# Optimization experiments

Measured on AMD Instinct MI355X. Metric: run time of the kernel, lower is better.

## Reference

```python
import jax, jax.numpy as jnp
import numpy as np

N_NODES = 20000   # num_of_nodes + 1 (incl. prediction node)
FEAT = 256        # in_features == hidden_features == out_features
N_LAYERS = 2
ALPHA = 0.2       # LeakyReLU negative slope
V_OBS = 512       # observed codes per patient
D_H = np.sqrt(FEAT * 1.0)  # sqrt(hidden_features * num_of_heads), n_heads=1
EPS = 1e-6


def _fc_edges(nodes):
    # torch: source = nodes.repeat(1, n); dest = each node repeated n times
    n = len(nodes)
    return np.stack([np.tile(nodes, n), np.repeat(nodes, n)]).astype(np.int64)


def setup_inputs() -> dict:
    key = jax.random.key(0)
    ks = jax.random.split(key, 16)
    rng = np.random.default_rng(0)
    obs = np.sort(rng.choice(np.arange(1, N_NODES - 1), size=V_OBS, replace=False))
    input_edges = jnp.asarray(_fc_edges(obs))
    obs_out = np.concatenate([obs, [N_NODES - 1]])  # add prediction node
    output_edges = jnp.asarray(_fc_edges(obs_out))

    s = 0.02
    embed = s * jax.random.normal(ks[0], (N_NODES, FEAT), jnp.float32)
    embed = embed.at[0].set(0.0)  # padding_idx=0
    return {
        "embed": embed,
        "W_w": s * jax.random.normal(ks[1], (N_LAYERS, FEAT, FEAT), jnp.float32),
        "W_b": s * jax.random.normal(ks[2], (N_LAYERS, FEAT), jnp.float32),
        "a": s * jax.random.normal(ks[3], (N_LAYERS, 2 * FEAT), jnp.float32),
        "ln_a": jnp.ones((N_LAYERS, FEAT), jnp.float32),
        "ln_b": jnp.zeros((N_LAYERS, FEAT), jnp.float32),
        "Wo_w": s * jax.random.normal(ks[4], (FEAT, FEAT), jnp.float32),
        "Wo_b": s * jax.random.normal(ks[5], (FEAT,), jnp.float32),
        "ao": s * jax.random.normal(ks[6], (2 * FEAT,), jnp.float32),
        "lno_a": jnp.ones((FEAT,), jnp.float32),
        "lno_b": jnp.zeros((FEAT,), jnp.float32),
        "lin_w": s * jax.random.normal(ks[7], (FEAT, FEAT), jnp.float32),
        "lin_b": s * jax.random.normal(ks[8], (FEAT,), jnp.float32),
        "param_w": s * jax.random.normal(ks[9], (2 * FEAT, FEAT), jnp.float32),
        "param_b": s * jax.random.normal(ks[10], (2 * FEAT,), jnp.float32),
        "out1_w": s * jax.random.normal(ks[11], (FEAT, FEAT), jnp.float32),
        "out1_b": s * jax.random.normal(ks[12], (FEAT,), jnp.float32),
        "out2_w": s * jax.random.normal(ks[13], (1, FEAT), jnp.float32),
        "out2_b": s * jax.random.normal(ks[14], (1,), jnp.float32),
        "input_edges": input_edges,
        "output_edges": output_edges,
    }


def _attention(x, edges, Ww, Wb, avec):
    # d = Linear(x): (N, H)
    d = x @ Ww.T + Wb
    H = d.shape[1]
    # a . [d_src ; d_dst] == (d @ a_left)[src] + (d @ a_right)[dst]  (cheaper, same math)
    s_node = d @ avec[:H]
    t_node = d @ avec[H:]
    score = s_node[edges[0]] + t_node[edges[1]]                  # (E,)
    e = jnp.exp(jax.nn.leaky_relu(score, ALPHA) / D_H)           # unnormalized attn
    n = x.shape[0]
    rowsum = jax.ops.segment_sum(e, edges[0], num_segments=n)   # (N,)
    agg = jax.ops.segment_sum(e[:, None] * d[edges[1]], edges[0], num_segments=n)
    zero = rowsum == 0
    # rows with no in-edges get an identity self-edge of weight 1 and rowsum 1
    agg = agg + jnp.where(zero[:, None], d, 0.0)
    return agg / jnp.where(zero, 1.0, rowsum)[:, None]


def _layernorm(x, g, b):
    m = x.mean(-1, keepdims=True)
    s = jnp.std(x, axis=-1, ddof=1, keepdims=True)  # torch std: unbiased
    return g * (x - m) / (s + EPS) + b


def reference(embed, W_w, W_b, a, ln_a, ln_b, Wo_w, Wo_b, ao, lno_a, lno_b,
              lin_w, lin_b, param_w, param_b, out1_w, out1_b, out2_w, out2_b,
              input_edges, output_edges):
    h = embed  # embedding lookup of arange(N) == the full table
    for l in range(N_LAYERS):  # in_att stack, concat=True, n_heads=1: ffn = LN -> ELU
        h = jax.nn.elu(_layernorm(_attention(h, input_edges, W_w[l], W_b[l], a[l]),
                                  ln_a[l], ln_b[l]))
    # variational layer (eval mode: reparameterize returns mu)
    hp = (h @ param_w.T + param_b).reshape(-1, 2, FEAT)
    h = hp[:, 0, :]  # mu
    # out_att: concat=False, mean over 1 head; ffn = LN -> ReLU -> Linear
    g = _attention(h, output_edges, Wo_w, Wo_b, ao)
    g = jax.nn.relu(_layernorm(g, lno_a, lno_b)) @ lin_w.T + lin_b
    # out_layer on prediction node: ReLU -> Linear -> ReLU -> Linear(->1)
    z = jax.nn.relu(g[-1])
    z = jax.nn.relu(z @ out1_w.T + out1_b)
    logit = z @ out2_w.T + out2_b  # (1,)
    return logit
```

## Files before the change

### kernel.cpp

```cpp
#include <hip/hip_runtime.h>
#include <hip/hip_bf16.h>

#define FEAT 256
#define NOBS 512
#define NOUT 513
#define GAT_ALPHA 0.2f
#define INV_DH (1.0f / 16.0f)
#define LN_EPS 1e-6f


__device__ __forceinline__ float b2f(unsigned short u) {
    union { float f; unsigned v; } x;
    x.v = ((unsigned)u) << 16;
    return x.f;
}

__device__ __forceinline__ float loadv(const void* p, long idx, int isbf) {
    if (isbf) return b2f(((const unsigned short*)p)[idx]);
    return ((const float*)p)[idx];
}

__device__ __forceinline__ float4 load4(const void* p, long idx, int isbf) {
    if (isbf) {
        ushort4 u = *(const ushort4*)((const unsigned short*)p + idx);
        return make_float4(b2f(u.x), b2f(u.y), b2f(u.z), b2f(u.w));
    }
    return *(const float4*)((const float*)p + idx);
}

__device__ __forceinline__ void detect(const void* w, const void* edges, int& isbf, int& estep) {
    const unsigned short* hb = (const unsigned short*)w;
    int sane = 0;
#pragma unroll
    for (int i = 0; i < 32; i += 2) {
        float a = fabsf(b2f(hb[i]));
        sane += (a > 1e-4f && a < 0.3f) ? 1 : 0;
    }
    isbf = (sane >= 8) ? 1 : 0;
    const int* ei = (const int*)edges;
    estep = (ei[1] == 0 && ei[3] == 0 && ei[5] == 0 && ei[7] == 0) ? 2 : 1;
}

__device__ __forceinline__ float wave_allreduce(float v) {
#pragma unroll
    for (int o = 1; o < 64; o <<= 1) v += __shfl_xor(v, o);
    return v;
}

__device__ __forceinline__ float block_sum256(float v, float* red) {
    __syncthreads();
    float s = v;
#pragma unroll
    for (int o = 32; o > 0; o >>= 1) s += __shfl_down(s, o);
    int lane = threadIdx.x & 63, wid = threadIdx.x >> 6;
    if (lane == 0) red[wid] = s;
    __syncthreads();
    return red[0] + red[1] + red[2] + red[3];
}

#define FV_AS0 0
#define FV_AS1 256
#define FV_AT0 512
#define FV_AT1 768
#define FV_WB0 1024
#define FV_WB1 1280
#define FV_LNA0 1536
#define FV_LNA1 1792
#define FV_LNB0 2048
#define FV_LNB1 2304
#define FV_WOB 2560
#define FV_AOS 2816
#define FV_AOT 3072
#define FV_LNOA 3328
#define FV_LNOB 3584
#define FV_LINB 3840
#define FV_PARB 4096
#define FV_O1B 4352
#define FV_O2W 4608
#define FV_O2B 4864

__global__ void k_prep(const void* embed, const void* W_w, const void* W_b, const void* a,
                       const void* ln_a, const void* ln_b, const void* Wo_w, const void* Wo_b,
                       const void* ao, const void* lno_a, const void* lno_b, const void* lin_w,
                       const void* lin_b, const void* param_w, const void* param_b,
                       const void* out1_w, const void* out1_b, const void* out2_w,
                       const void* out2_b, const void* oedges,
                       float* fv, float* packs, float* X, int* flags) {
    int isbf, estep;
    detect(W_w, oedges, isbf, estep);
    int b = blockIdx.x, tid = threadIdx.x;
    if (b < 96) {
        __shared__ float tile[64][65];
        int m = b >> 4, t = b & 15;
        int f0 = (t >> 2) << 6, k0 = (t & 3) << 6;
        const void* base;
        long eoff = 0;
        switch (m) {
            case 0: base = W_w; break;
            case 1: base = W_w; eoff = 65536; break;
            case 2: base = param_w; break;
            case 3: base = Wo_w; break;
            case 4: base = lin_w; break;
            default: base = out1_w; break;
        }
        int r = tid >> 2, cq = (tid & 3) << 4;
#pragma unroll
        for (int jj = 0; jj < 4; jj++) {
            float4 v = load4(base, eoff + (long)(f0 + r) * FEAT + k0 + cq + (jj << 2), isbf);
            tile[r][cq + (jj << 2) + 0] = v.x;
            tile[r][cq + (jj << 2) + 1] = v.y;
            tile[r][cq + (jj << 2) + 2] = v.z;
            tile[r][cq + (jj << 2) + 3] = v.w;
        }
        __syncthreads();
        int w = tid >> 6, lane = tid & 63;
        float4* pack = (float4*)(packs + (long)m * 65536);
#pragma unroll
        for (int it = 0; it < 4; it++) {
            int kk = ((w << 2) + it) << 2;
            float4 v = make_float4(tile[lane][kk], tile[lane][kk + 1],
                                   tile[lane][kk + 2], tile[lane][kk + 3]);
            int k4g = (k0 >> 2) + (w << 2) + it;
            pack[(k4g << 8) + f0 + lane] = v;
        }
    } else if (b < 96 + NOUT) {
        int i = b - 96;
        const int* oe = (const int*)oedges;
        long node = oe[(long)i * estep];
        X[(long)i * FEAT + tid] = loadv(embed, node * FEAT + tid, isbf);
    } else {
        int cid = b - 96 - NOUT;
        const void* s;
        long so = 0;
        float* d;
        int n = 256;
        switch (cid) {
            case 0:  s = a;       so = 0;   d = fv + FV_AS0;  break;
            case 1:  s = a;       so = 512; d = fv + FV_AS1;  break;
            case 2:  s = a;       so = 256; d = fv + FV_AT0;  break;
            case 3:  s = a;       so = 768; d = fv + FV_AT1;  break;
            case 4:  s = W_b;     so = 0;   d = fv + FV_WB0;  break;
            case 5:  s = W_b;     so = 256; d = fv + FV_WB1;  break;
            case 6:  s = ln_a;    so = 0;   d = fv + FV_LNA0; break;
            case 7:  s = ln_a;    so = 256; d = fv + FV_LNA1; break;
            case 8:  s = ln_b;    so = 0;   d = fv + FV_LNB0; break;
            case 9:  s = ln_b;    so = 256; d = fv + FV_LNB1; break;
            case 10: s = Wo_b;    so = 0;   d = fv + FV_WOB;  break;
            case 11: s = ao;      so = 0;   d = fv + FV_AOS;  break;
            case 12: s = ao;      so = 256; d = fv + FV_AOT;  break;
            case 13: s = lno_a;   so = 0;   d = fv + FV_LNOA; break;
            case 14: s = lno_b;   so = 0;   d = fv + FV_LNOB; break;
            case 15: s = lin_b;   so = 0;   d = fv + FV_LINB; break;
            case 16: s = param_b; so = 0;   d = fv + FV_PARB; break;
            case 17: s = out1_b;  so = 0;   d = fv + FV_O1B;  break;
            case 18: s = out2_w;  so = 0;   d = fv + FV_O2W;  break;
            default: s = out2_b;  so = 0;   d = fv + FV_O2B;  n = 1; break;
        }
        for (int idx = tid; idx < n; idx += FEAT) d[idx] = loadv(s, so + idx, isbf);
        if (cid == 19 && tid == 0) { flags[0] = isbf; flags[1] = estep; }
    }
}

template <bool WITH_ST, bool PWO>
__global__ void k_dense(const float* __restrict__ X, const float4* __restrict__ W1,
                        const float* __restrict__ b1, const float4* __restrict__ W2,
                        const float* __restrict__ b2v, const float* __restrict__ as_,
                        const float* __restrict__ at_, float* __restrict__ D,
                        float* S, float* T) {
    __shared__ __align__(16) float4 xs4[4][64];
    __shared__ __align__(16) float dsh[4][FEAT];
    int tid = threadIdx.x, lane = tid & 63, w = tid >> 6;
    int i0 = blockIdx.x << 2;
    int nr = NOUT - i0;
    if (nr > 4) nr = 4;
    if (w < nr) xs4[w][lane] = ((const float4*)(X + (long)(i0 + w) * FEAT))[lane];
    __syncthreads();
    float acc[4] = {0.f, 0.f, 0.f, 0.f};
#pragma unroll 4
    for (int k4 = 0; k4 < 64; k4++) {
        float4 wv = W1[(k4 << 8) + tid];
#pragma unroll
        for (int r = 0; r < 4; r++) {
            float4 xv = xs4[r][k4];
            acc[r] += xv.x * wv.x + xv.y * wv.y + xv.z * wv.z + xv.w * wv.w;
        }
    }
    float bb = b1[tid];
#pragma unroll
    for (int r = 0; r < 4; r++) acc[r] += bb;
    if (PWO) {
#pragma unroll
        for (int r = 0; r < 4; r++) dsh[r][tid] = acc[r];
        __syncthreads();
        float acc2[4] = {0.f, 0.f, 0.f, 0.f};
#pragma unroll 4
        for (int k4 = 0; k4 < 64; k4++) {
            float4 wv = W2[(k4 << 8) + tid];
#pragma unroll
            for (int r = 0; r < 4; r++) {
                float4 xv = ((const float4*)dsh[r])[k4];
                acc2[r] += xv.x * wv.x + xv.y * wv.y + xv.z * wv.z + xv.w * wv.w;
            }
        }
        float b2 = b2v[tid];
#pragma unroll
        for (int r = 0; r < 4; r++) acc[r] = acc2[r] + b2;
    }
#pragma unroll
    for (int r = 0; r < 4; r++)
        if (r < nr) D[(long)(i0 + r) * FEAT + tid] = acc[r];
    if (WITH_ST) {
        __syncthreads();
#pragma unroll
        for (int r = 0; r < 4; r++) dsh[r][tid] = acc[r];
        __syncthreads();
        if (w < nr) {
            float sv = 0.f, tv = 0.f;
#pragma unroll
            for (int q = 0; q < 4; q++) {
                float dv = dsh[w][lane + (q << 6)];
                sv += dv * as_[lane + (q << 6)];
                tv += dv * at_[lane + (q << 6)];
            }
            sv = wave_allreduce(sv);
            tv = wave_allreduce(tv);
            if (lane == 0) { S[i0 + w] = sv; T[i0 + w] = tv; }
        }
    }
}

__global__ void k_attn(const float* __restrict__ D, const float* __restrict__ S,
                       const float* __restrict__ T, const float* __restrict__ ga,
                       const float* __restrict__ gb, float* __restrict__ Xout) {
    __shared__ __align__(16) float e[4][NOBS];
    __shared__ __align__(16) float sacc[4][4][FEAT];
    __shared__ float rs[4];
    __shared__ float red[8];
    int tid = threadIdx.x, lane = tid & 63, w = tid >> 6;
    int bi = blockIdx.x;
    if (bi < 128) {
        int i0 = bi << 2;
#pragma unroll
        for (int r = 0; r < 4; r++) {
            float si = S[i0 + r];
#pragma unroll
            for (int h = 0; h < 2; h++) {
                int j = tid + (h << 8);
                float sc = si + T[j];
                sc = (sc > 0.f ? sc : GAT_ALPHA * sc) * INV_DH;
                e[r][j] = __expf(sc);
            }
        }
        __syncthreads();
        float p = 0.f;
#pragma unroll
        for (int q = 0; q < 8; q++) p += e[w][lane + (q << 6)];
        p = wave_allreduce(p);
        if (lane == 0) rs[w] = p;
        float4 a0 = make_float4(0.f, 0.f, 0.f, 0.f), a1 = a0, a2 = a0, a3 = a0;
#pragma unroll 4
        for (int jj = 0; jj < 128; jj++) {
            int j = (jj << 2) | w;
            float4 dv = *(const float4*)(D + (long)j * FEAT + (lane << 2));
            float e0 = e[0][j], e1 = e[1][j], e2 = e[2][j], e3 = e[3][j];
            a0.x += e0 * dv.x; a0.y += e0 * dv.y; a0.z += e0 * dv.z; a0.w += e0 * dv.w;
            a1.x += e1 * dv.x; a1.y += e1 * dv.y; a1.z += e1 * dv.z; a1.w += e1 * dv.w;
            a2.x += e2 * dv.x; a2.y += e2 * dv.y; a2.z += e2 * dv.z; a2.w += e2 * dv.w;
            a3.x += e3 * dv.x; a3.y += e3 * dv.y; a3.z += e3 * dv.z; a3.w += e3 * dv.w;
        }
        *(float4*)&sacc[w][0][lane << 2] = a0;
        *(float4*)&sacc[w][1][lane << 2] = a1;
        *(float4*)&sacc[w][2][lane << 2] = a2;
        *(float4*)&sacc[w][3][lane << 2] = a3;
        __syncthreads();
        float inv_rs = 1.f / rs[w];
        float v[4], m = 0.f;
#pragma unroll
        for (int q = 0; q < 4; q++) {
            int f = lane + (q << 6);
            v[q] = (sacc[0][w][f] + sacc[1][w][f] + sacc[2][w][f] + sacc[3][w][f]) * inv_rs;
            m += v[q];
        }
        m = wave_allreduce(m) * (1.f / FEAT);
        float var = 0.f;
#pragma unroll
        for (int q = 0; q < 4; q++) { v[q] -= m; var += v[q] * v[q]; }
        var = wave_allreduce(var) * (1.f / (FEAT - 1));
        float isd = 1.f / (sqrtf(var) + LN_EPS);
#pragma unroll
        for (int q = 0; q < 4; q++) {
            int f = lane + (q << 6);
            float y = ga[f] * v[q] * isd + gb[f];
            Xout[(long)(i0 + w) * FEAT + f] = (y > 0.f) ? y : (__expf(y) - 1.f);
        }
    } else {
        float val = D[(long)NOBS * FEAT + tid];
        float m = block_sum256(val, red) * (1.f / FEAT);
        float dv = val - m;
        float var = block_sum256(dv * dv, red) * (1.f / (FEAT - 1));
        float y = ga[tid] * dv / (sqrtf(var) + LN_EPS) + gb[tid];
        Xout[(long)NOBS * FEAT + tid] = (y > 0.f) ? y : (__expf(y) - 1.f);
    }
}

__global__ void k_aggout(const float* __restrict__ D, const float* __restrict__ S,
                         const float* __restrict__ T, float* partial, float* prsum) {
    __shared__ float es[16];
    __shared__ __align__(16) float wacc[4][FEAT];
    int tid = threadIdx.x, lane = tid & 63, w = tid >> 6;
    int b = blockIdx.x;
    float sN = S[NOUT - 1];
    if (b == 32) {
        float sc = sN + T[NOUT - 1];
        sc = (sc > 0.f ? sc : GAT_ALPHA * sc) * INV_DH;
        float ev = __expf(sc);
        partial[(long)b * FEAT + tid] = ev * D[(long)(NOUT - 1) * FEAT + tid];
        if (tid == 0) prsum[b] = ev;
        return;
    }
    int j0 = b << 4;
    if (tid < 16) {
        float sc = sN + T[j0 + tid];
        sc = (sc > 0.f ? sc : GAT_ALPHA * sc) * INV_DH;
        es[tid] = __expf(sc);
    }
    __syncthreads();
    float4 acc = make_float4(0.f, 0.f, 0.f, 0.f);
#pragma unroll
    for (int q = 0; q < 4; q++) {
        int jl = (w << 2) + q;
        float ev = es[jl];
        float4 dv = *(const float4*)(D + (long)(j0 + jl) * FEAT + (lane << 2));
        acc.x += ev * dv.x; acc.y += ev * dv.y;
        acc.z += ev * dv.z; acc.w += ev * dv.w;
    }
    *(float4*)&wacc[w][lane << 2] = acc;
    __syncthreads();
    partial[(long)b * FEAT + tid] = wacc[0][tid] + wacc[1][tid] + wacc[2][tid] + wacc[3][tid];
    if (tid == 0) {
        float s = 0.f;
#pragma unroll
        for (int q = 0; q < 16; q++) s += es[q];
        prsum[b] = s;
    }
}

__global__ void k_head(const float* __restrict__ partial, const float* __restrict__ prsum,
                       const float* __restrict__ lnoA, const float* __restrict__ lnoB,
                       const float4* __restrict__ linP, const float* __restrict__ linB,
                       const float4* __restrict__ o1P, const float* __restrict__ o1B,
                       const float* __restrict__ o2w, const float* __restrict__ o2b,
                       const int* flags, void* out) {
    __shared__ float red[8];
    __shared__ __align__(16) float ys[FEAT];
    __shared__ __align__(16) float zs[FEAT];
    int tid = threadIdx.x;
    float val = 0.f;
#pragma unroll
    for (int b = 0; b < 33; b++) val += partial[(b << 8) + tid];
    float rssum = 0.f;
#pragma unroll
    for (int b = 0; b < 33; b++) rssum += prsum[b];
    val /= rssum;
    float m = block_sum256(val, red) * (1.f / FEAT);
    float dv = val - m;
    float var = block_sum256(dv * dv, red) * (1.f / (FEAT - 1));
    float y = lnoA[tid] * dv / (sqrtf(var) + LN_EPS) + lnoB[tid];
    ys[tid] = fmaxf(y, 0.f);
    __syncthreads();
    float g = 0.f;
#pragma unroll 8
    for (int k4 = 0; k4 < 64; k4++) {
        float4 wv = linP[(k4 << 8) + tid];
        float4 yv = ((const float4*)ys)[k4];
        g += yv.x * wv.x + yv.y * wv.y + yv.z * wv.z + yv.w * wv.w;
    }
    g += linB[tid];
    zs[tid] = fmaxf(g, 0.f);
    __syncthreads();
    float z2 = 0.f;
#pragma unroll 8
    for (int k4 = 0; k4 < 64; k4++) {
        float4 wv = o1P[(k4 << 8) + tid];
        float4 zv = ((const float4*)zs)[k4];
        z2 += zv.x * wv.x + zv.y * wv.y + zv.z * wv.z + zv.w * wv.w;
    }
    z2 = fmaxf(z2 + o1B[tid], 0.f);
    float logit = block_sum256(z2 * o2w[tid], red) + o2b[0];
    if (tid == 0) {
        if (flags[0]) ((__hip_bfloat16*)out)[0] = __float2bfloat16(logit);
        else ((float*)out)[0] = logit;
    }
}

extern "C" void kernel_launch(void* const* d_in, const int* in_sizes, int n_in,
                              void* d_out, int out_size, void* d_ws, size_t ws_size,
                              hipStream_t stream) {
    const void* embed = d_in[0];
    const void* W_w = d_in[1];
    const void* W_b = d_in[2];
    const void* a = d_in[3];
    const void* ln_a = d_in[4];
    const void* ln_b = d_in[5];
    const void* Wo_w = d_in[6];
    const void* Wo_b = d_in[7];
    const void* ao = d_in[8];
    const void* lno_a = d_in[9];
    const void* lno_b = d_in[10];
    const void* lin_w = d_in[11];
    const void* lin_b = d_in[12];
    const void* param_w = d_in[13];
    const void* param_b = d_in[14];
    const void* out1_w = d_in[15];
    const void* out1_b = d_in[16];
    const void* out2_w = d_in[17];
    const void* out2_b = d_in[18];
    const void* oedges = d_in[20];

    char* ws = (char*)d_ws;
    int* flags = (int*)ws;
    float* fv = (float*)(ws + 256);
    float* packs = (float*)(ws + 32768);
    float* X = (float*)(ws + 1605632);
    float* D = (float*)(ws + 2134016);
    float* S = (float*)(ws + 2662400);
    float* T = (float*)(ws + 2666496);
    float* partial = (float*)(ws + 2670592);
    float* prsum = (float*)(ws + 2707456);

    const float4* P0 = (const float4*)(packs + 0 * 65536);
    const float4* P1 = (const float4*)(packs + 1 * 65536);
    const float4* PP = (const float4*)(packs + 2 * 65536);
    const float4* PWo = (const float4*)(packs + 3 * 65536);
    const float4* PL = (const float4*)(packs + 4 * 65536);
    const float4* PO1 = (const float4*)(packs + 5 * 65536);

    k_prep<<<96 + NOUT + 20, FEAT, 0, stream>>>(embed, W_w, W_b, a, ln_a, ln_b, Wo_w, Wo_b,
                                                ao, lno_a, lno_b, lin_w, lin_b, param_w,
                                                param_b, out1_w, out1_b, out2_w, out2_b,
                                                oedges, fv, packs, X, flags);
    k_dense<true, false><<<129, FEAT, 0, stream>>>(X, P0, fv + FV_WB0, nullptr, nullptr,
                                                   fv + FV_AS0, fv + FV_AT0, D, S, T);
    k_attn<<<129, FEAT, 0, stream>>>(D, S, T, fv + FV_LNA0, fv + FV_LNB0, X);
    k_dense<true, false><<<129, FEAT, 0, stream>>>(X, P1, fv + FV_WB1, nullptr, nullptr,
                                                   fv + FV_AS1, fv + FV_AT1, D, S, T);
    k_attn<<<129, FEAT, 0, stream>>>(D, S, T, fv + FV_LNA1, fv + FV_LNB1, X);
    k_dense<true, true><<<129, FEAT, 0, stream>>>(X, PP, fv + FV_PARB, PWo, fv + FV_WOB,
                                                  fv + FV_AOS, fv + FV_AOT, D, S, T);
    k_aggout<<<33, FEAT, 0, stream>>>(D, S, T, partial, prsum);
    k_head<<<1, FEAT, 0, stream>>>(partial, prsum, fv + FV_LNOA, fv + FV_LNOB, PL,
                                   fv + FV_LINB, PO1, fv + FV_O1B, fv + FV_O2W,
                                   fv + FV_O2B, flags, d_out);
}
```

Baseline: 111.2 us.

## Fuse all stages into one persistent kernel with grid-wide atomic barriers

Replaces the eight separate kernel launches (prep, dense, attention, aggregation, head) with one persistent 129-block kernel. The stages are separated by a hand-rolled grid barrier built from atomics and a spin-wait. This is meant to remove per-launch overhead and the gaps between dependent kernels in a workload dominated by small launches. It adds a memset for the barrier counters and relies on all 129 blocks being co-resident, which risks deadlock if they are not. Prep work is now spread over fewer blocks, and idle blocks spin at each barrier.

```diff
diff --git a/kernel.cpp b/kernel.cpp
--- a/kernel.cpp
+++ b/kernel.cpp
@@ -4,6 +4,7 @@
 #define FEAT 256
 #define NOBS 512
 #define NOUT 513
+#define NBLK 129
 #define GAT_ALPHA 0.2f
 #define INV_DH (1.0f / 16.0f)
 #define LN_EPS 1e-6f
@@ -56,6 +57,18 @@
     if (lane == 0) red[wid] = s;
     __syncthreads();
     return red[0] + red[1] + red[2] + red[3];
+}
+
+__device__ __forceinline__ void gsync(int* bar, int idx) {
+    __syncthreads();
+    if (threadIdx.x == 0) {
+        __threadfence();
+        atomicAdd(&bar[idx], 1);
+        while (__hip_atomic_load(&bar[idx], __ATOMIC_RELAXED, __HIP_MEMORY_SCOPE_AGENT) < NBLK)
+            __builtin_amdgcn_s_sleep(2);
+        __threadfence();
+    }
+    __syncthreads();
 }
 
 #define FV_AS0 0
@@ -79,96 +92,14 @@
 #define FV_O2W 4608
 #define FV_O2B 4864
 
-__global__ void k_prep(const void* embed, const void* W_w, const void* W_b, const void* a,
-                       const void* ln_a, const void* ln_b, const void* Wo_w, const void* Wo_b,
-                       const void* ao, const void* lno_a, const void* lno_b, const void* lin_w,
-                       const void* lin_b, const void* param_w, const void* param_b,
-                       const void* out1_w, const void* out1_b, const void* out2_w,
-                       const void* out2_b, const void* oedges,
-                       float* fv, float* packs, float* X, int* flags) {
-    int isbf, estep;
-    detect(W_w, oedges, isbf, estep);
-    int b = blockIdx.x, tid = threadIdx.x;
-    if (b < 96) {
-        __shared__ float tile[64][65];
-        int m = b >> 4, t = b & 15;
-        int f0 = (t >> 2) << 6, k0 = (t & 3) << 6;
-        const void* base;
-        long eoff = 0;
-        switch (m) {
-            case 0: base = W_w; break;
-            case 1: base = W_w; eoff = 65536; break;
-            case 2: base = param_w; break;
-            case 3: base = Wo_w; break;
-            case 4: base = lin_w; break;
-            default: base = out1_w; break;
-        }
-        int r = tid >> 2, cq = (tid & 3) << 4;
-#pragma unroll
-        for (int jj = 0; jj < 4; jj++) {
-            float4 v = load4(base, eoff + (long)(f0 + r) * FEAT + k0 + cq + (jj << 2), isbf);
-            tile[r][cq + (jj << 2) + 0] = v.x;
-            tile[r][cq + (jj << 2) + 1] = v.y;
-            tile[r][cq + (jj << 2) + 2] = v.z;
-            tile[r][cq + (jj << 2) + 3] = v.w;
-        }
-        __syncthreads();
-        int w = tid >> 6, lane = tid & 63;
-        float4* pack = (float4*)(packs + (long)m * 65536);
-#pragma unroll
-        for (int it = 0; it < 4; it++) {
-            int kk = ((w << 2) + it) << 2;
-            float4 v = make_float4(tile[lane][kk], tile[lane][kk + 1],
-                                   tile[lane][kk + 2], tile[lane][kk + 3]);
-            int k4g = (k0 >> 2) + (w << 2) + it;
-            pack[(k4g << 8) + f0 + lane] = v;
-        }
-    } else if (b < 96 + NOUT) {
-        int i = b - 96;
-        const int* oe = (const int*)oedges;
-        long node = oe[(long)i * estep];
-        X[(long)i * FEAT + tid] = loadv(embed, node * FEAT + tid, isbf);
-    } else {
-        int cid = b - 96 - NOUT;
-        const void* s;
-        long so = 0;
-        float* d;
-        int n = 256;
-        switch (cid) {
-            case 0:  s = a;       so = 0;   d = fv + FV_AS0;  break;
-            case 1:  s = a;       so = 512; d = fv + FV_AS1;  break;
-            case 2:  s = a;       so = 256; d = fv + FV_AT0;  break;
-            case 3:  s = a;       so = 768; d = fv + FV_AT1;  break;
-            case 4:  s = W_b;     so = 0;   d = fv + FV_WB0;  break;
-            case 5:  s = W_b;     so = 256; d = fv + FV_WB1;  break;
-            case 6:  s = ln_a;    so = 0;   d = fv + FV_LNA0; break;
-            case 7:  s = ln_a;    so = 256; d = fv + FV_LNA1; break;
-            case 8:  s = ln_b;    so = 0;   d = fv + FV_LNB0; break;
-            case 9:  s = ln_b;    so = 256; d = fv + FV_LNB1; break;
-            case 10: s = Wo_b;    so = 0;   d = fv + FV_WOB;  break;
-            case 11: s = ao;      so = 0;   d = fv + FV_AOS;  break;
-            case 12: s = ao;      so = 256; d = fv + FV_AOT;  break;
-            case 13: s = lno_a;   so = 0;   d = fv + FV_LNOA; break;
-            case 14: s = lno_b;   so = 0;   d = fv + FV_LNOB; break;
-            case 15: s = lin_b;   so = 0;   d = fv + FV_LINB; break;
-            case 16: s = param_b; so = 0;   d = fv + FV_PARB; break;
-            case 17: s = out1_b;  so = 0;   d = fv + FV_O1B;  break;
-            case 18: s = out2_w;  so = 0;   d = fv + FV_O2W;  break;
-            default: s = out2_b;  so = 0;   d = fv + FV_O2B;  n = 1; break;
-        }
-        for (int idx = tid; idx < n; idx += FEAT) d[idx] = loadv(s, so + idx, isbf);
-        if (cid == 19 && tid == 0) { flags[0] = isbf; flags[1] = estep; }
-    }
-}
-
-template <bool WITH_ST, bool PWO>
-__global__ void k_dense(const float* __restrict__ X, const float4* __restrict__ W1,
-                        const float* __restrict__ b1, const float4* __restrict__ W2,
-                        const float* __restrict__ b2v, const float* __restrict__ as_,
-                        const float* __restrict__ at_, float* __restrict__ D,
-                        float* S, float* T) {
-    __shared__ __align__(16) float4 xs4[4][64];
-    __shared__ __align__(16) float dsh[4][FEAT];
+template <bool PWO>
+__device__ __forceinline__ void dense_stage(char* smem, const float* __restrict__ X,
+        const float4* __restrict__ W1, const float* __restrict__ b1,
+        const float4* __restrict__ W2, const float* __restrict__ b2v,
+        const float* __restrict__ as_, const float* __restrict__ at_,
+        float* __restrict__ D, float* S, float* T) {
+    float4 (*xs4)[64] = (float4(*)[64])smem;
+    float (*dsh)[FEAT] = (float(*)[FEAT])(smem + 4096);
     int tid = threadIdx.x, lane = tid & 63, w = tid >> 6;
     int i0 = blockIdx.x << 2;
     int nr = NOUT - i0;
@@ -209,33 +140,31 @@
 #pragma unroll
     for (int r = 0; r < 4; r++)
         if (r < nr) D[(long)(i0 + r) * FEAT + tid] = acc[r];
-    if (WITH_ST) {
-        __syncthreads();
-#pragma unroll
-        for (int r = 0; r < 4; r++) dsh[r][tid] = acc[r];
-        __syncthreads();
-        if (w < nr) {
-            float sv = 0.f, tv = 0.f;
-#pragma unroll
-            for (int q = 0; q < 4; q++) {
-                float dv = dsh[w][lane + (q << 6)];
-                sv += dv * as_[lane + (q << 6)];
-                tv += dv * at_[lane + (q << 6)];
-            }
-            sv = wave_allreduce(sv);
-            tv = wave_allreduce(tv);
-            if (lane == 0) { S[i0 + w] = sv; T[i0 + w] = tv; }
-        }
-    }
-}
-
-__global__ void k_attn(const float* __restrict__ D, const float* __restrict__ S,
-                       const float* __restrict__ T, const float* __restrict__ ga,
-                       const float* __restrict__ gb, float* __restrict__ Xout) {
-    __shared__ __align__(16) float e[4][NOBS];
-    __shared__ __align__(16) float sacc[4][4][FEAT];
-    __shared__ float rs[4];
-    __shared__ float red[8];
+    __syncthreads();
+#pragma unroll
+    for (int r = 0; r < 4; r++) dsh[r][tid] = acc[r];
+    __syncthreads();
+    if (w < nr) {
+        float sv = 0.f, tv = 0.f;
+#pragma unroll
+        for (int q = 0; q < 4; q++) {
+            float dv = dsh[w][lane + (q << 6)];
+            sv += dv * as_[lane + (q << 6)];
+            tv += dv * at_[lane + (q << 6)];
+        }
+        sv = wave_allreduce(sv);
+        tv = wave_allreduce(tv);
+        if (lane == 0) { S[i0 + w] = sv; T[i0 + w] = tv; }
+    }
+}
+
+__device__ __forceinline__ void attn_stage(char* smem, const float* __restrict__ D,
+        const float* __restrict__ S, const float* __restrict__ T,
+        const float* __restrict__ ga, const float* __restrict__ gb, float* __restrict__ Xout) {
+    float (*e)[NOBS] = (float(*)[NOBS])smem;
+    float (*sacc)[4][FEAT] = (float(*)[4][FEAT])(smem + 8192);
+    float* red = (float*)(smem + 24576);
+    float* rs = (float*)(smem + 24608);
     int tid = threadIdx.x, lane = tid & 63, w = tid >> 6;
     int bi = blockIdx.x;
     if (bi < 128) {
@@ -303,93 +232,192 @@
     }
 }
 
-__global__ void k_aggout(const float* __restrict__ D, const float* __restrict__ S,
-                         const float* __restrict__ T, float* partial, float* prsum) {
-    __shared__ float es[16];
-    __shared__ __align__(16) float wacc[4][FEAT];
-    int tid = threadIdx.x, lane = tid & 63, w = tid >> 6;
-    int b = blockIdx.x;
-    float sN = S[NOUT - 1];
-    if (b == 32) {
-        float sc = sN + T[NOUT - 1];
-        sc = (sc > 0.f ? sc : GAT_ALPHA * sc) * INV_DH;
-        float ev = __expf(sc);
-        partial[(long)b * FEAT + tid] = ev * D[(long)(NOUT - 1) * FEAT + tid];
-        if (tid == 0) prsum[b] = ev;
-        return;
-    }
-    int j0 = b << 4;
-    if (tid < 16) {
-        float sc = sN + T[j0 + tid];
-        sc = (sc > 0.f ? sc : GAT_ALPHA * sc) * INV_DH;
-        es[tid] = __expf(sc);
-    }
-    __syncthreads();
-    float4 acc = make_float4(0.f, 0.f, 0.f, 0.f);
-#pragma unroll
-    for (int q = 0; q < 4; q++) {
-        int jl = (w << 2) + q;
-        float ev = es[jl];
-        float4 dv = *(const float4*)(D + (long)(j0 + jl) * FEAT + (lane << 2));
-        acc.x += ev * dv.x; acc.y += ev * dv.y;
-        acc.z += ev * dv.z; acc.w += ev * dv.w;
-    }
-    *(float4*)&wacc[w][lane << 2] = acc;
-    __syncthreads();
-    partial[(long)b * FEAT + tid] = wacc[0][tid] + wacc[1][tid] + wacc[2][tid] + wacc[3][tid];
-    if (tid == 0) {
-        float s = 0.f;
-#pragma unroll
-        for (int q = 0; q < 16; q++) s += es[q];
-        prsum[b] = s;
-    }
-}
-
-__global__ void k_head(const float* __restrict__ partial, const float* __restrict__ prsum,
-                       const float* __restrict__ lnoA, const float* __restrict__ lnoB,
-                       const float4* __restrict__ linP, const float* __restrict__ linB,
-                       const float4* __restrict__ o1P, const float* __restrict__ o1B,
-                       const float* __restrict__ o2w, const float* __restrict__ o2b,
-                       const int* flags, void* out) {
-    __shared__ float red[8];
-    __shared__ __align__(16) float ys[FEAT];
-    __shared__ __align__(16) float zs[FEAT];
-    int tid = threadIdx.x;
-    float val = 0.f;
-#pragma unroll
-    for (int b = 0; b < 33; b++) val += partial[(b << 8) + tid];
-    float rssum = 0.f;
-#pragma unroll
-    for (int b = 0; b < 33; b++) rssum += prsum[b];
-    val /= rssum;
-    float m = block_sum256(val, red) * (1.f / FEAT);
-    float dv = val - m;
-    float var = block_sum256(dv * dv, red) * (1.f / (FEAT - 1));
-    float y = lnoA[tid] * dv / (sqrtf(var) + LN_EPS) + lnoB[tid];
-    ys[tid] = fmaxf(y, 0.f);
-    __syncthreads();
-    float g = 0.f;
+__global__ __launch_bounds__(256, 1) void k_mega(
+        const void* embed, const void* W_w, const void* W_b, const void* a,
+        const void* ln_a, const void* ln_b, const void* Wo_w, const void* Wo_b,
+        const void* ao, const void* lno_a, const void* lno_b, const void* lin_w,
+        const void* lin_b, const void* param_w, const void* param_b,
+        const void* out1_w, const void* out1_b, const void* out2_w, const void* out2_b,
+        const void* oedges, int* bar, float* fv, float* packs, float* X, float* D,
+        float* S, float* T, float* partial, float* prsum, void* out) {
+    __shared__ __align__(16) char smem[25088];
+    int tid = threadIdx.x, lane = tid & 63, w = tid >> 6, b = blockIdx.x;
+    int isbf, estep;
+    detect(W_w, oedges, isbf, estep);
+
+    const float4* P0 = (const float4*)(packs + 0 * 65536);
+    const float4* P1 = (const float4*)(packs + 1 * 65536);
+    const float4* PP = (const float4*)(packs + 2 * 65536);
+    const float4* PWo = (const float4*)(packs + 3 * 65536);
+    const float4* PL = (const float4*)(packs + 4 * 65536);
+    const float4* PO1 = (const float4*)(packs + 5 * 65536);
+
+    for (int job = b; job < 96 + NOUT + 20; job += NBLK) {
+        if (job < 96) {
+            float (*tile)[65] = (float(*)[65])smem;
+            int m = job >> 4, t = job & 15;
+            int f0 = (t >> 2) << 6, k0 = (t & 3) << 6;
+            const void* base;
+            long eoff = 0;
+            switch (m) {
+                case 0: base = W_w; break;
+                case 1: base = W_w; eoff = 65536; break;
+                case 2: base = param_w; break;
+                case 3: base = Wo_w; break;
+                case 4: base = lin_w; break;
+                default: base = out1_w; break;
+            }
+            int r = tid >> 2, cq = (tid & 3) << 4;
+#pragma unroll
+            for (int jj = 0; jj < 4; jj++) {
+                float4 v = load4(base, eoff + (long)(f0 + r) * FEAT + k0 + cq + (jj << 2), isbf);
+                tile[r][cq + (jj << 2) + 0] = v.x;
+                tile[r][cq + (jj << 2) + 1] = v.y;
+                tile[r][cq + (jj << 2) + 2] = v.z;
+                tile[r][cq + (jj << 2) + 3] = v.w;
+            }
+            __syncthreads();
+            float4* pack = (float4*)(packs + (long)m * 65536);
+#pragma unroll
+            for (int it = 0; it < 4; it++) {
+                int kk = ((w << 2) + it) << 2;
+                float4 v = make_float4(tile[lane][kk], tile[lane][kk + 1],
+                                       tile[lane][kk + 2], tile[lane][kk + 3]);
+                int k4g = (k0 >> 2) + (w << 2) + it;
+                pack[(k4g << 8) + f0 + lane] = v;
+            }
+        } else if (job < 96 + NOUT) {
+            int i = job - 96;
+            const int* oe = (const int*)oedges;
+            long node = oe[(long)i * estep];
+            X[(long)i * FEAT + tid] = loadv(embed, node * FEAT + tid, isbf);
+        } else {
+            int cid = job - 96 - NOUT;
+            const void* s;
+            long so = 0;
+            float* d;
+            int n = 256;
+            switch (cid) {
+                case 0:  s = a;       so = 0;   d = fv + FV_AS0;  break;
+                case 1:  s = a;       so = 512; d = fv + FV_AS1;  break;
+                case 2:  s = a;       so = 256; d = fv + FV_AT0;  break;
+                case 3:  s = a;       so = 768; d = fv + FV_AT1;  break;
+                case 4:  s = W_b;     so = 0;   d = fv + FV_WB0;  break;
+                case 5:  s = W_b;     so = 256; d = fv + FV_WB1;  break;
+                case 6:  s = ln_a;    so = 0;   d = fv + FV_LNA0; break;
+                case 7:  s = ln_a;    so = 256; d = fv + FV_LNA1; break;
+                case 8:  s = ln_b;    so = 0;   d = fv + FV_LNB0; break;
+                case 9:  s = ln_b;    so = 256; d = fv + FV_LNB1; break;
+                case 10: s = Wo_b;    so = 0;   d = fv + FV_WOB;  break;
+                case 11: s = ao;      so = 0;   d = fv + FV_AOS;  break;
+                case 12: s = ao;      so = 256; d = fv + FV_AOT;  break;
+                case 13: s = lno_a;   so = 0;   d = fv + FV_LNOA; break;
+                case 14: s = lno_b;   so = 0;   d = fv + FV_LNOB; break;
+                case 15: s = lin_b;   so = 0;   d = fv + FV_LINB; break;
+                case 16: s = param_b; so = 0;   d = fv + FV_PARB; break;
+                case 17: s = out1_b;  so = 0;   d = fv + FV_O1B;  break;
+                case 18: s = out2_w;  so = 0;   d = fv + FV_O2W;  break;
+                default: s = out2_b;  so = 0;   d = fv + FV_O2B;  n = 1; break;
+            }
+            for (int idx = tid; idx < n; idx += FEAT) d[idx] = loadv(s, so + idx, isbf);
+        }
+    }
+    gsync(bar, 0);
+
+    dense_stage<false>(smem, X, P0, fv + FV_WB0, nullptr, nullptr,
+                       fv + FV_AS0, fv + FV_AT0, D, S, T);
+    gsync(bar, 1);
+    attn_stage(smem, D, S, T, fv + FV_LNA0, fv + FV_LNB0, X);
+    gsync(bar, 2);
+    dense_stage<false>(smem, X, P1, fv + FV_WB1, nullptr, nullptr,
+                       fv + FV_AS1, fv + FV_AT1, D, S, T);
+    gsync(bar, 3);
+    attn_stage(smem, D, S, T, fv + FV_LNA1, fv + FV_LNB1, X);
+    gsync(bar, 4);
+    dense_stage<true>(smem, X, PP, fv + FV_PARB, PWo, fv + FV_WOB,
+                      fv + FV_AOS, fv + FV_AOT, D, S, T);
+    gsync(bar, 5);
+
+    if (b < 33) {
+        float* es = (float*)smem;
+        float (*wacc)[FEAT] = (float(*)[FEAT])(smem + 64);
+        float sN = S[NOUT - 1];
+        if (b == 32) {
+            float sc = sN + T[NOUT - 1];
+            sc = (sc > 0.f ? sc : GAT_ALPHA * sc) * INV_DH;
+            float ev = __expf(sc);
+            partial[(long)b * FEAT + tid] = ev * D[(long)(NOUT - 1) * FEAT + tid];
+            if (tid == 0) prsum[b] = ev;
+        } else {
+            int j0 = b << 4;
+            if (tid < 16) {
+                float sc = sN + T[j0 + tid];
+                sc = (sc > 0.f ? sc : GAT_ALPHA * sc) * INV_DH;
+                es[tid] = __expf(sc);
+            }
+            __syncthreads();
+            float4 acc = make_float4(0.f, 0.f, 0.f, 0.f);
+#pragma unroll
+            for (int q = 0; q < 4; q++) {
+                int jl = (w << 2) + q;
+                float ev = es[jl];
+                float4 dv = *(const float4*)(D + (long)(j0 + jl) * FEAT + (lane << 2));
+                acc.x += ev * dv.x; acc.y += ev * dv.y;
+                acc.z += ev * dv.z; acc.w += ev * dv.w;
+            }
+            *(float4*)&wacc[w][lane << 2] = acc;
+            __syncthreads();
+            partial[(long)b * FEAT + tid] = wacc[0][tid] + wacc[1][tid] + wacc[2][tid] + wacc[3][tid];
+            if (tid == 0) {
+                float s = 0.f;
+#pragma unroll
+                for (int q = 0; q < 16; q++) s += es[q];
+                prsum[b] = s;
+            }
+        }
+    }
+    gsync(bar, 6);
+
+    if (b == 0) {
+        float* red = (float*)smem;
+        float* ys = (float*)(smem + 64);
+        float* zs = (float*)(smem + 64 + 1024);
+        float val = 0.f;
+#pragma unroll
+        for (int p = 0; p < 33; p++) val += partial[(p << 8) + tid];
+        float rssum = 0.f;
+#pragma unroll
+        for (int p = 0; p < 33; p++) rssum += prsum[p];
+        val /= rssum;
+        float m = block_sum256(val, red) * (1.f / FEAT);
+        float dv = val - m;
+        float var = block_sum256(dv * dv, red) * (1.f / (FEAT - 1));
+        float y = fv[FV_LNOA + tid] * dv / (sqrtf(var) + LN_EPS) + fv[FV_LNOB + tid];
+        ys[tid] = fmaxf(y, 0.f);
+        __syncthreads();
+        float g = 0.f;
 #pragma unroll 8
-    for (int k4 = 0; k4 < 64; k4++) {
-        float4 wv = linP[(k4 << 8) + tid];
-        float4 yv = ((const float4*)ys)[k4];
-        g += yv.x * wv.x + yv.y * wv.y + yv.z * wv.z + yv.w * wv.w;
-    }
-    g += linB[tid];
-    zs[tid] = fmaxf(g, 0.f);
-    __syncthreads();
-    float z2 = 0.f;
+        for (int k4 = 0; k4 < 64; k4++) {
+            float4 wv = PL[(k4 << 8) + tid];
+            float4 yv = ((const float4*)ys)[k4];
+            g += yv.x * wv.x + yv.y * wv.y + yv.z * wv.z + yv.w * wv.w;
+        }
+        g += fv[FV_LINB + tid];
+        zs[tid] = fmaxf(g, 0.f);
+        __syncthreads();
+        float z2 = 0.f;
 #pragma unroll 8
-    for (int k4 = 0; k4 < 64; k4++) {
-        float4 wv = o1P[(k4 << 8) + tid];
-        float4 zv = ((const float4*)zs)[k4];
-        z2 += zv.x * wv.x + zv.y * wv.y + zv.z * wv.z + zv.w * wv.w;
-    }
-    z2 = fmaxf(z2 + o1B[tid], 0.f);
-    float logit = block_sum256(z2 * o2w[tid], red) + o2b[0];
-    if (tid == 0) {
-        if (flags[0]) ((__hip_bfloat16*)out)[0] = __float2bfloat16(logit);
-        else ((float*)out)[0] = logit;
+        for (int k4 = 0; k4 < 64; k4++) {
+            float4 wv = PO1[(k4 << 8) + tid];
+            float4 zv = ((const float4*)zs)[k4];
+            z2 += zv.x * wv.x + zv.y * wv.y + zv.z * wv.z + zv.w * wv.w;
+        }
+        z2 = fmaxf(z2 + fv[FV_O1B + tid], 0.f);
+        float logit = block_sum256(z2 * fv[FV_O2W + tid], red) + fv[FV_O2B];
+        if (tid == 0) {
+            if (isbf) ((__hip_bfloat16*)out)[0] = __float2bfloat16(logit);
+            else ((float*)out)[0] = logit;
+        }
     }
 }
 
@@ -418,7 +446,7 @@
     const void* oedges = d_in[20];
 
     char* ws = (char*)d_ws;
-    int* flags = (int*)ws;
+    int* bar = (int*)ws;
     float* fv = (float*)(ws + 256);
     float* packs = (float*)(ws + 32768);
     float* X = (float*)(ws + 1605632);
@@ -426,29 +454,11 @@
     float* S = (float*)(ws + 2662400);
     float* T = (float*)(ws + 2666496);
     float* partial = (float*)(ws + 2670592);
-    float* prsum = (float*)(ws + 2707456);
-
-    const float4* P0 = (const float4*)(packs + 0 * 65536);
-    const float4* P1 = (const float4*)(packs + 1 * 65536);
-    const float4* PP = (const float4*)(packs + 2 * 65536);
-    const float4* PWo = (const float4*)(packs + 3 * 65536);
-    const float4* PL = (const float4*)(packs + 4 * 65536);
-    const float4* PO1 = (const float4*)(packs + 5 * 65536);
-
-    k_prep<<<96 + NOUT + 20, FEAT, 0, stream>>>(embed, W_w, W_b, a, ln_a, ln_b, Wo_w, Wo_b,
-                                                ao, lno_a, lno_b, lin_w, lin_b, param_w,
-                                                param_b, out1_w, out1_b, out2_w, out2_b,
-                                                oedges, fv, packs, X, flags);
-    k_dense<true, false><<<129, FEAT, 0, stream>>>(X, P0, fv + FV_WB0, nullptr, nullptr,
-                                                   fv + FV_AS0, fv + FV_AT0, D, S, T);
-    k_attn<<<129, FEAT, 0, stream>>>(D, S, T, fv + FV_LNA0, fv + FV_LNB0, X);
-    k_dense<true, false><<<129, FEAT, 0, stream>>>(X, P1, fv + FV_WB1, nullptr, nullptr,
-                                                   fv + FV_AS1, fv + FV_AT1, D, S, T);
-    k_attn<<<129, FEAT, 0, stream>>>(D, S, T, fv + FV_LNA1, fv + FV_LNB1, X);
-    k_dense<true, true><<<129, FEAT, 0, stream>>>(X, PP, fv + FV_PARB, PWo, fv + FV_WOB,
-                                                  fv + FV_AOS, fv + FV_AOT, D, S, T);
-    k_aggout<<<33, FEAT, 0, stream>>>(D, S, T, partial, prsum);
-    k_head<<<1, FEAT, 0, stream>>>(partial, prsum, fv + FV_LNOA, fv + FV_LNOB, PL,
-                                   fv + FV_LINB, PO1, fv + FV_O1B, fv + FV_O2W,
-                                   fv + FV_O2B, flags, d_out);
-}
+    float* prsum = (float*)(ws + 2704384);
+
+    hipMemsetAsync(bar, 0, 64, stream);
+    k_mega<<<NBLK, FEAT, 0, stream>>>(embed, W_w, W_b, a, ln_a, ln_b, Wo_w, Wo_b, ao,
+                                      lno_a, lno_b, lin_w, lin_b, param_w, param_b,
+                                      out1_w, out1_b, out2_w, out2_b, oedges,
+                                      bar, fv, packs, X, D, S, T, partial, prsum, d_out);
+}
```

Result: slower. 148.2 us (+33.3%).
